# Optimization experiments

Measured on AMD Instinct MI355X. Metric: run time of the kernel, lower is better.

## Reference

```python
import jax, jax.numpy as jnp
import numpy as np

N, E, C, D, H = 50000, 1600000, 50000, 128, 512


def setup_inputs() -> dict:
    key = jax.random.key(0)
    ks = jax.random.split(key, 16)
    s = jnp.float32(0.02)  # keep activations stable through 3 layers
    inp = {}
    inp["x"] = jax.random.normal(ks[0], (N, D), jnp.float32)
    inp["edge_index"] = jax.random.randint(ks[1], (2, E), 0, N)
    inp["first_edge"] = jax.random.randint(ks[2], (2,), 0, N)
    inp["candidate_edges"] = jax.random.randint(ks[3], (C, 2), 0, N)
    inp["t"] = jax.random.uniform(ks[4], (1, 1), jnp.float32)
    dims = [(D, H), (H, H), (H, H)]
    i = 5
    for l, (di, do) in enumerate(dims):
        inp[f"gin{l}_w1"] = jax.random.normal(ks[i], (di, do), jnp.float32) * s; i += 1
        inp[f"gin{l}_b1"] = jnp.zeros((do,), jnp.float32)
        inp[f"gin{l}_w2"] = jax.random.normal(ks[i], (do, do), jnp.float32) * s; i += 1
        inp[f"gin{l}_b2"] = jnp.zeros((do,), jnp.float32)
    inp["pred_w1"] = jax.random.normal(ks[i], (5 * H, H), jnp.float32) * s; i += 1
    inp["pred_b1"] = jnp.zeros((H,), jnp.float32)
    inp["pred_w2"] = jax.random.normal(ks[i], (H, 1), jnp.float32) * s; i += 1
    inp["pred_b2"] = jnp.zeros((1,), jnp.float32)
    inp["time_w1"] = jax.random.normal(ks[i], (1, H), jnp.float32) * s; i += 1
    inp["time_b1"] = jnp.zeros((H,), jnp.float32)
    inp["time_w2"] = jax.random.normal(ks[i], (H, H), jnp.float32) * s; i += 1
    inp["time_b2"] = jnp.zeros((H,), jnp.float32)
    return inp


def _edge_rep(x, u, v):
    # 'sum_absdiff': cat([x_u + x_v, |x_u - x_v|]) -> 2*H features
    xu, xv = x[u], x[v]
    return jnp.concatenate([xu + xv, jnp.abs(xu - xv)], axis=-1)


def reference(x, edge_index, first_edge, candidate_edges, t,
              gin0_w1, gin0_b1, gin0_w2, gin0_b2,
              gin1_w1, gin1_b1, gin1_w2, gin1_b2,
              gin2_w1, gin2_b1, gin2_w2, gin2_b2,
              pred_w1, pred_b1, pred_w2, pred_b2,
              time_w1, time_b1, time_w2, time_b2):
    src, dst = edge_index[0], edge_index[1]
    layers = [(gin0_w1, gin0_b1, gin0_w2, gin0_b2),
              (gin1_w1, gin1_b1, gin1_w2, gin1_b2),
              (gin2_w1, gin2_b1, gin2_w2, gin2_b2)]
    # GINConv (eps=0): h_i = MLP(x_i + sum_{j->i} x_j)
    for w1, b1, w2, b2 in layers:
        agg = jax.ops.segment_sum(x[src], dst, num_segments=x.shape[0])
        h = x + agg
        x = jax.nn.relu(h @ w1 + b1) @ w2 + b2
    first_feat = _edge_rep(x, first_edge[0], first_edge[1])  # [2H]
    t_embed = (jax.nn.relu(t @ time_w1 + time_b1) @ time_w2 + time_b2)[0]  # [H]
    cand_feat = _edge_rep(x, candidate_edges[:, 0], candidate_edges[:, 1])  # [C, 2H]
    Cn = cand_feat.shape[0]
    feat = jnp.concatenate([
        jnp.broadcast_to(first_feat, (Cn, first_feat.shape[0])),
        cand_feat,
        jnp.broadcast_to(t_embed, (Cn, t_embed.shape[0])),
    ], axis=-1)  # [C, 5H]
    logits = (jax.nn.relu(feat @ pred_w1 + pred_b1) @ pred_w2 + pred_b2)[:, 0]  # [C]
    return logits
```

## Files before the change

kernel.cpp:

```cpp
#include <hip/hip_runtime.h>

typedef __bf16 bf16x2 __attribute__((ext_vector_type(2)));
typedef __bf16 bf16x4 __attribute__((ext_vector_type(4)));
typedef __bf16 bf16x8 __attribute__((ext_vector_type(8)));
typedef float f32x4 __attribute__((ext_vector_type(4)));

#define CSR_CHUNKS 256

__device__ __forceinline__ void gload16(const __bf16* g, __bf16* l) {
    __builtin_amdgcn_global_load_lds((const __attribute__((address_space(1))) void*)g,
                                     (__attribute__((address_space(3))) void*)l, 16, 0, 0);
}

__global__ __launch_bounds__(256)
void hist_part_kernel(const int* __restrict__ dst, int* __restrict__ deg, int E, int N) {
    const int r = blockIdx.x & 7;
    const int chunk = blockIdx.x >> 3;
    const int RS = (N + 7) >> 3;
    const int lo = r * RS;
    const int hi = min(lo + RS, N);
    const int stride = CSR_CHUNKS * 256;
    for (int i = chunk * 256 + threadIdx.x; i < E; i += stride) {
        int d = dst[i];
        if (d >= lo && d < hi) atomicAdd(&deg[d], 1);
    }
}

__global__ __launch_bounds__(256)
void scatter_part_kernel(const int* __restrict__ src, const int* __restrict__ dst,
                         int* __restrict__ cursor, int* __restrict__ colsrc, int E, int N) {
    const int r = blockIdx.x & 7;
    const int chunk = blockIdx.x >> 3;
    const int RS = (N + 7) >> 3;
    const int lo = r * RS;
    const int hi = min(lo + RS, N);
    const int stride = CSR_CHUNKS * 256;
    for (int i = chunk * 256 + threadIdx.x; i < E; i += stride) {
        int d = dst[i];
        if (d >= lo && d < hi) {
            int p = atomicAdd(&cursor[d], 1);
            colsrc[p] = src[i];
        }
    }
}

__global__ __launch_bounds__(256)
void blocksum_kernel(const int* __restrict__ deg, int* __restrict__ bsum, int n) {
    __shared__ int red[256];
    int i = blockIdx.x * 256 + threadIdx.x;
    red[threadIdx.x] = (i < n) ? deg[i] : 0;
    __syncthreads();
    for (int off = 128; off > 0; off >>= 1) {
        if (threadIdx.x < off) red[threadIdx.x] += red[threadIdx.x + off];
        __syncthreads();
    }
    if (threadIdx.x == 0) bsum[blockIdx.x] = red[0];
}

__global__ __launch_bounds__(256)
void scanb_kernel(int* __restrict__ bsum, int nb) {
    __shared__ int s[256];
    int t = threadIdx.x;
    s[t] = (t < nb) ? bsum[t] : 0;
    __syncthreads();
    for (int off = 1; off < 256; off <<= 1) {
        int v = (t >= off) ? s[t - off] : 0;
        __syncthreads();
        s[t] += v;
        __syncthreads();
    }
    if (t < nb) bsum[t] = (t == 0) ? 0 : s[t - 1];
}

__global__ __launch_bounds__(256)
void scanw_kernel(const int* __restrict__ deg, const int* __restrict__ bsum,
                  int* __restrict__ rowptr, int* __restrict__ cursor, int n) {
    __shared__ int s[256];
    int b = blockIdx.x, t = threadIdx.x;
    int i = b * 256 + t;
    int d = (i < n) ? deg[i] : 0;
    s[t] = d;
    __syncthreads();
    for (int off = 1; off < 256; off <<= 1) {
        int v = (t >= off) ? s[t - off] : 0;
        __syncthreads();
        s[t] += v;
        __syncthreads();
    }
    int incl = s[t];
    int base = bsum[b];
    if (i < n) {
        int r = base + incl - d;
        rowptr[i] = r;
        cursor[i] = r;
        if (i == n - 1) rowptr[n] = base + incl;
    }
}

__global__ void f32_to_bf16_kernel(const float* __restrict__ in, __bf16* __restrict__ out, int n4) {
    int i = blockIdx.x * 256 + threadIdx.x;
    if (i < n4) {
        float4 f = ((const float4*)in)[i];
        bf16x4 o;
        o[0] = (__bf16)f.x; o[1] = (__bf16)f.y; o[2] = (__bf16)f.z; o[3] = (__bf16)f.w;
        ((bf16x4*)out)[i] = o;
    }
}

__global__ void wprep_kernel(const float* __restrict__ in, __bf16* __restrict__ out, int kbits) {
    int idx = blockIdx.x * 256 + threadIdx.x;
    int K = 1 << kbits;
    if (idx < (512 << kbits)) {
        int k = idx & (K - 1);
        int n = idx >> kbits;
        out[idx] = (__bf16)in[k * 512 + n];
    }
}

template<int F> struct VecT;
template<> struct VecT<2> { using T = bf16x2; };
template<> struct VecT<4> { using T = bf16x4; };
template<> struct VecT<8> { using T = bf16x8; };

template<int F, int U, int STR>
__global__ __launch_bounds__(256)
void agg_kernel(const __bf16* __restrict__ xb, const int* __restrict__ rowptr,
                const int* __restrict__ colsrc, __bf16* __restrict__ h, int n, int colbase) {
    const int node = blockIdx.x * 4 + (threadIdx.x >> 6);
    if (node >= n) return;
    const int lane = threadIdx.x & 63;
    using V = typename VecT<F>::T;

    const __bf16* xl = xb + colbase + lane * F;

    float acc[F];
    {
        V v = *(const V*)(xl + (size_t)node * STR);
        #pragma unroll
        for (int i = 0; i < F; i++) acc[i] = (float)v[i];
    }

    int e   = __builtin_amdgcn_readfirstlane(rowptr[node]);
    int end = __builtin_amdgcn_readfirstlane(rowptr[node + 1]);

    for (; e + U <= end; e += U) {
        int s[U];
        #pragma unroll
        for (int j = 0; j < U; j++) s[j] = colsrc[e + j];
        V v[U];
        #pragma unroll
        for (int j = 0; j < U; j++) v[j] = *(const V*)(xl + (size_t)s[j] * STR);
        #pragma unroll
        for (int j = 0; j < U; j++)
            #pragma unroll
            for (int i = 0; i < F; i++) acc[i] += (float)v[j][i];
    }
    if constexpr (U > 4) {
        for (; e + 4 <= end; e += 4) {
            int s[4];
            #pragma unroll
            for (int j = 0; j < 4; j++) s[j] = colsrc[e + j];
            V v[4];
            #pragma unroll
            for (int j = 0; j < 4; j++) v[j] = *(const V*)(xl + (size_t)s[j] * STR);
            #pragma unroll
            for (int j = 0; j < 4; j++)
                #pragma unroll
                for (int i = 0; i < F; i++) acc[i] += (float)v[j][i];
        }
    }
    for (; e < end; e++) {
        int s0 = colsrc[e];
        V v = *(const V*)(xl + (size_t)s0 * STR);
        #pragma unroll
        for (int i = 0; i < F; i++) acc[i] += (float)v[i];
    }

    __bf16* out = h + colbase + (size_t)node * STR + lane * F;
    V o;
    #pragma unroll
    for (int i = 0; i < F; i++) o[i] = (__bf16)acc[i];
    *(V*)out = o;
}

template<bool RELU>
__global__ __launch_bounds__(512, 1)
void gemmF_kernel(const __bf16* __restrict__ A, const __bf16* __restrict__ Bt,
                  const float* __restrict__ bias, __bf16* __restrict__ Cout,
                  int M, int K) {
    __shared__ __bf16 smem[36864];
    __bf16* const sA0 = smem;
    __bf16* const sA1 = smem + 2048;
    __bf16* const sB0 = smem + 4096;
    __bf16* const sB1 = smem + 20480;

    const int tid = threadIdx.x;
    const int lane = tid & 63;
    const int wid = tid >> 6;
    const int mlane = lane & 15;
    const int quad = lane >> 4;
    const int rowBase = blockIdx.x * 64;

    const int swzc = (((lane & 3) ^ ((lane >> 3) & 3)) << 3);

    const int aRow = rowBase + wid * 16 + (lane >> 2);
    const int aRowC = (aRow < M) ? aRow : (M - 1);
    const __bf16* aSrc = A + (size_t)aRowC * K + swzc;
    const int bRow = wid * 64 + (lane >> 2);
    const __bf16* bSrc = Bt + (size_t)bRow * K + swzc;

    const int rkey = (mlane >> 1) & 3;
    const int base_r = mlane * 32 + ((quad ^ rkey) << 3);

    f32x4 acc[4][4];
    #pragma unroll
    for (int i = 0; i < 4; i++)
        #pragma unroll
        for (int j = 0; j < 4; j++) acc[i][j] = f32x4{0.f, 0.f, 0.f, 0.f};

    auto stage = [&](__bf16* bufA, __bf16* bufB, int k0) {
        if (wid < 4) gload16(aSrc + k0, bufA + wid * 512);
        #pragma unroll
        for (int j = 0; j < 4; j++)
            gload16(bSrc + (size_t)j * 16 * K + k0, bufB + wid * 2048 + j * 512);
    };
    auto waitc = [&]() {
        if (wid < 4) { asm volatile("s_waitcnt vmcnt(5)" ::: "memory"); }
        else         { asm volatile("s_waitcnt vmcnt(4)" ::: "memory"); }
    };
    auto compute = [&](const __bf16* bufA, const __bf16* bufB) {
        bf16x8 aF[4], bF[4];
        #pragma unroll
        for (int mt = 0; mt < 4; mt++)
            aF[mt] = *(const bf16x8*)(bufA + mt * 512 + base_r);
        #pragma unroll
        for (int nt = 0; nt < 4; nt++)
            bF[nt] = *(const bf16x8*)(bufB + wid * 2048 + nt * 512 + base_r);
        #pragma unroll
        for (int mt = 0; mt < 4; mt++)
            #pragma unroll
            for (int nt = 0; nt < 4; nt++)
                acc[mt][nt] = __builtin_amdgcn_mfma_f32_16x16x32_bf16(aF[mt], bF[nt], acc[mt][nt], 0, 0, 0);
    };

    const int nt = K >> 5;
    stage(sA0, sB0, 0);
    __builtin_amdgcn_sched_barrier(0);
    stage(sA1, sB1, 32);
    waitc();
    __builtin_amdgcn_sched_barrier(0);
    __builtin_amdgcn_s_barrier();
    __builtin_amdgcn_sched_barrier(0);

    int cur = 0;
    for (int t = 0; t < nt; ++t) {
        __bf16* cA = cur ? sA1 : sA0;
        __bf16* cB = cur ? sB1 : sB0;
        compute(cA, cB);
        if (t + 1 < nt) {
            __builtin_amdgcn_s_barrier();
            __builtin_amdgcn_sched_barrier(0);
            if (t + 2 < nt) {
                stage(cA, cB, (t + 2) << 5);
                waitc();
            } else {
                asm volatile("s_waitcnt vmcnt(0)" ::: "memory");
            }
            __builtin_amdgcn_sched_barrier(0);
            __builtin_amdgcn_s_barrier();
            __builtin_amdgcn_sched_barrier(0);
            cur ^= 1;
        }
    }

    float bv[4];
    #pragma unroll
    for (int nt2 = 0; nt2 < 4; nt2++) bv[nt2] = bias[wid * 64 + nt2 * 16 + mlane];

    float* tp = (float*)smem;
    const int erow = tid >> 5;
    const int ecg = tid & 31;
    #pragma unroll
    for (int mt = 0; mt < 4; mt++) {
        __syncthreads();
        #pragma unroll
        for (int nt2 = 0; nt2 < 4; nt2++) {
            #pragma unroll
            for (int r = 0; r < 4; r++) {
                float v = acc[mt][nt2][r] + bv[nt2];
                if (RELU) v = fmaxf(v, 0.f);
                tp[(quad * 4 + r) * 520 + wid * 64 + nt2 * 16 + mlane] = v;
            }
        }
        __syncthreads();
        int gr = rowBase + mt * 16 + erow;
        if (gr < M) {
            const float* rp = tp + erow * 520 + ecg * 16;
            f32x4 a = *(const f32x4*)(rp);
            f32x4 b = *(const f32x4*)(rp + 4);
            f32x4 c = *(const f32x4*)(rp + 8);
            f32x4 d = *(const f32x4*)(rp + 12);
            bf16x8 o0, o1;
            #pragma unroll
            for (int j = 0; j < 4; j++) { o0[j] = (__bf16)a[j]; o0[4 + j] = (__bf16)b[j]; }
            #pragma unroll
            for (int j = 0; j < 4; j++) { o1[j] = (__bf16)c[j]; o1[4 + j] = (__bf16)d[j]; }
            __bf16* op = Cout + (size_t)gr * 512 + ecg * 16;
            *(bf16x8*)op = o0;
            *(bf16x8*)(op + 8) = o1;
        }
    }
}

template<int AMODE, bool RELU>
__global__ __launch_bounds__(256, 3)
void gemm_kernel(const __bf16* __restrict__ A, const __bf16* __restrict__ Xb,
                 const int* __restrict__ cand, const __bf16* __restrict__ Bt,
                 const float* __restrict__ bias, __bf16* __restrict__ Cout,
                 int M, int K) {
    __shared__ __bf16 smem[2 * (2048 + 8192)];
    __bf16* const sA0 = smem;
    __bf16* const sA1 = smem + 2048;
    __bf16* const sB0 = smem + 4096;
    __bf16* const sB1 = smem + 4096 + 8192;

    const int bx = blockIdx.x;
    const int rblk = (bx >> 4) * 8 + (bx & 7);
    const int panel = (bx >> 3) & 1;
    const int rowBase = rblk * 64;
    if (rowBase >= M) return;
    const int nBase = panel * 256;

    const int tid = threadIdx.x;
    const int lane = tid & 63;
    const int wid = tid >> 6;
    const int mlane = lane & 15;
    const int quad = lane >> 4;

    const int swzc = (((lane & 3) ^ ((lane >> 3) & 3)) << 3);
    const int bRow = nBase + wid * 64 + (lane >> 2);
    const __bf16* bSrc = Bt + (size_t)bRow * K + swzc;

    const int rkey = (mlane >> 1) & 3;
    const int base_r = mlane * 32 + ((quad ^ rkey) << 3);

    const int ar = tid >> 2;
    const int acn = tid & 3;
    const int ac = acn << 3;
    const int wkey = (ar >> 1) & 3;
    const int woffA = ar * 32 + ((acn ^ wkey) << 3);

    f32x4 acc[4][4];
    #pragma unroll
    for (int i = 0; i < 4; i++)
        #pragma unroll
        for (int j = 0; j < 4; j++) acc[i][j] = f32x4{0.f, 0.f, 0.f, 0.f};

    int uu = 0, vv = 0;
    const int grow = rowBase + ar;
    const bool arowok = (grow < M);
    if (AMODE == 1 && arowok) { uu = cand[2 * grow]; vv = cand[2 * grow + 1]; }

    bf16x8 pxu{}, pxv{};
    int pk = 0;

    auto stageB = [&](__bf16* bufB, int k0) {
        #pragma unroll
        for (int j = 0; j < 4; j++)
            gload16(bSrc + (size_t)j * 16 * K + k0, bufB + wid * 2048 + j * 512);
    };
    auto issueA1 = [&](int k0) {
        pk = k0;
        if (arowok) {
            int kk = (k0 + ac) & 511;
            pxu = *(const bf16x8*)(Xb + (size_t)uu * 512 + kk);
            pxv = *(const bf16x8*)(Xb + (size_t)vv * 512 + kk);
        }
    };
    auto commitA1 = [&](__bf16* bufA) {
        bf16x8 av = bf16x8{};
        if (arowok) {
            if (pk + ac < 512) {
                #pragma unroll
                for (int q = 0; q < 8; q++) av[q] = (__bf16)((float)pxu[q] + (float)pxv[q]);
            } else {
                #pragma unroll
                for (int q = 0; q < 8; q++) av[q] = (__bf16)fabsf((float)pxu[q] - (float)pxv[q]);
            }
        }
        *(bf16x8*)(bufA + woffA) = av;
    };

    auto compute = [&](const __bf16* bufA, const __bf16* bufB) {
        bf16x8 aF[4], bF[4];
        #pragma unroll
        for (int mt = 0; mt < 4; mt++)
            aF[mt] = *(const bf16x8*)(bufA + mt * 512 + base_r);
        #pragma unroll
        for (int nt = 0; nt < 4; nt++)
            bF[nt] = *(const bf16x8*)(bufB + wid * 2048 + nt * 512 + base_r);
        #pragma unroll
        for (int mt = 0; mt < 4; mt++)
            #pragma unroll
            for (int nt = 0; nt < 4; nt++)
                acc[mt][nt] = __builtin_amdgcn_mfma_f32_16x16x32_bf16(aF[mt], bF[nt], acc[mt][nt], 0, 0, 0);
    };

    const int nt = K >> 5;
    issueA1(0);
    commitA1(sA0);
    stageB(sB0, 0);
    __syncthreads();
    for (int t = 0; t < nt; t += 2) {
        issueA1((t + 1) << 5);
        stageB(sB1, (t + 1) << 5);
        compute(sA0, sB0);
        commitA1(sA1);
        __syncthreads();
        if (t + 2 < nt) {
            issueA1((t + 2) << 5);
            stageB(sB0, (t + 2) << 5);
        }
        compute(sA1, sB1);
        if (t + 2 < nt) commitA1(sA0);
        __syncthreads();
    }

    float bv[4];
    #pragma unroll
    for (int nt2 = 0; nt2 < 4; nt2++) bv[nt2] = bias[nBase + wid * 64 + nt2 * 16 + mlane];

    float* tp = (float*)smem;
    const int erow = tid >> 4;
    const int ecg = tid & 15;
    #pragma unroll
    for (int mt = 0; mt < 4; mt++) {
        __syncthreads();
        #pragma unroll
        for (int nt2 = 0; nt2 < 4; nt2++) {
            #pragma unroll
            for (int r = 0; r < 4; r++) {
                float v = acc[mt][nt2][r] + bv[nt2];
                if (RELU) v = fmaxf(v, 0.f);
                tp[(quad * 4 + r) * 260 + wid * 64 + nt2 * 16 + mlane] = v;
            }
        }
        __syncthreads();
        int gr = rowBase + mt * 16 + erow;
        if (gr < M) {
            const float* rp = tp + erow * 260 + ecg * 16;
            f32x4 a = *(const f32x4*)(rp);
            f32x4 b = *(const f32x4*)(rp + 4);
            f32x4 c = *(const f32x4*)(rp + 8);
            f32x4 d = *(const f32x4*)(rp + 12);
            bf16x8 o0, o1;
            #pragma unroll
            for (int j = 0; j < 4; j++) { o0[j] = (__bf16)a[j]; o0[4 + j] = (__bf16)b[j]; }
            #pragma unroll
            for (int j = 0; j < 4; j++) { o1[j] = (__bf16)c[j]; o1[4 + j] = (__bf16)d[j]; }
            __bf16* op = Cout + (size_t)gr * 512 + nBase + ecg * 16;
            *(bf16x8*)op = o0;
            *(bf16x8*)(op + 8) = o1;
        }
    }
}

__global__ __launch_bounds__(512)
void constvec_kernel(const __bf16* __restrict__ xb, const int* __restrict__ first_edge,
                     const float* __restrict__ t,
                     const float* __restrict__ tw1, const float* __restrict__ tb1,
                     const float* __restrict__ tw2, const float* __restrict__ tb2,
                     const float* __restrict__ pw1, const float* __restrict__ pb1,
                     float* __restrict__ cvec) {
    __shared__ float z1[512];
    __shared__ float te[512];
    __shared__ float ff[1024];
    int tid = threadIdx.x;
    float tv = t[0];
    z1[tid] = fmaxf(tv * tw1[tid] + tb1[tid], 0.f);
    int u = first_edge[0], v = first_edge[1];
    float xu = (float)xb[(size_t)u * 512 + tid];
    float xv = (float)xb[(size_t)v * 512 + tid];
    ff[tid] = xu + xv;
    ff[512 + tid] = fabsf(xu - xv);
    __syncthreads();
    float s = tb2[tid];
    for (int j = 0; j < 512; j++) s += z1[j] * tw2[j * 512 + tid];
    te[tid] = s;
    __syncthreads();
    float c = pb1[tid];
    for (int k = 0; k < 1024; k++) c += ff[k] * pw1[k * 512 + tid];
    for (int j = 0; j < 512; j++) c += te[j] * pw1[(2048 + j) * 512 + tid];
    cvec[tid] = c;
}

__global__ __launch_bounds__(256)
void logits_kernel(const __bf16* __restrict__ Z, const float* __restrict__ w2,
                   const float* __restrict__ b2, float* __restrict__ out, int C) {
    int c = blockIdx.x * 4 + (threadIdx.x >> 6);
    if (c >= C) return;
    int lane = threadIdx.x & 63;
    bf16x8 z = *(const bf16x8*)(Z + (size_t)c * 512 + lane * 8);
    const float4* w = (const float4*)(w2 + lane * 8);
    float4 w0 = w[0], w1 = w[1];
    float s = (float)z[0] * w0.x + (float)z[1] * w0.y + (float)z[2] * w0.z + (float)z[3] * w0.w
            + (float)z[4] * w1.x + (float)z[5] * w1.y + (float)z[6] * w1.z + (float)z[7] * w1.w;
    #pragma unroll
    for (int off = 32; off > 0; off >>= 1) s += __shfl_down(s, off);
    if (lane == 0) out[c] = s + b2[0];
}

extern "C" void kernel_launch(void* const* d_in, const int* in_sizes, int n_in,
                              void* d_out, int out_size, void* d_ws, size_t ws_size,
                              hipStream_t stream) {
    (void)n_in; (void)out_size; (void)ws_size;
    const float* x          = (const float*)d_in[0];
    const int*   edge_index = (const int*)d_in[1];
    const int*   first_edge = (const int*)d_in[2];
    const int*   cand       = (const int*)d_in[3];
    const float* t          = (const float*)d_in[4];
    const float* gw1[3] = {(const float*)d_in[5], (const float*)d_in[9],  (const float*)d_in[13]};
    const float* gb1[3] = {(const float*)d_in[6], (const float*)d_in[10], (const float*)d_in[14]};
    const float* gw2[3] = {(const float*)d_in[7], (const float*)d_in[11], (const float*)d_in[15]};
    const float* gb2[3] = {(const float*)d_in[8], (const float*)d_in[12], (const float*)d_in[16]};
    const float* pw1 = (const float*)d_in[17];
    const float* pb1 = (const float*)d_in[18];
    const float* pw2 = (const float*)d_in[19];
    const float* pb2 = (const float*)d_in[20];
    const float* tw1 = (const float*)d_in[21];
    const float* tb1 = (const float*)d_in[22];
    const float* tw2 = (const float*)d_in[23];
    const float* tb2 = (const float*)d_in[24];

    const int N = in_sizes[0] / 128;
    const int E = in_sizes[1] / 2;
    const int C = in_sizes[3] / 2;

    char* p = (char*)d_ws;
    auto alloc = [&](size_t bytes) -> void* {
        void* r = (void*)p;
        p += (bytes + 255) & ~(size_t)255;
        return r;
    };
    __bf16* h    = (__bf16*)alloc((size_t)N * 512 * 2);
    __bf16* u    = (__bf16*)alloc((size_t)N * 512 * 2);
    __bf16* xb   = (__bf16*)alloc((size_t)N * 512 * 2);
    __bf16* wt01 = (__bf16*)alloc((size_t)512 * 128 * 2);
    __bf16* wt02 = (__bf16*)alloc((size_t)512 * 512 * 2);
    __bf16* wt11 = (__bf16*)alloc((size_t)512 * 512 * 2);
    __bf16* wt12 = (__bf16*)alloc((size_t)512 * 512 * 2);
    __bf16* wt21 = (__bf16*)alloc((size_t)512 * 512 * 2);
    __bf16* wt22 = (__bf16*)alloc((size_t)512 * 512 * 2);
    __bf16* wtH  = (__bf16*)alloc((size_t)512 * 1024 * 2);
    int* rowptr = (int*)alloc((size_t)(N + 1) * 4);
    int* deg    = (int*)alloc((size_t)N * 4);
    int* cursor = (int*)alloc((size_t)N * 4);
    int* colsrc = (int*)alloc((size_t)E * 4);
    int* bsum   = (int*)alloc((size_t)256 * 4);
    float* cvec = (float*)alloc(512 * 4);
    __bf16* xb0 = (__bf16*)u;

    const int* src = edge_index;
    const int* dst = edge_index + E;

    hipMemsetAsync(deg, 0, (size_t)N * 4, stream);
    int nb = (N + 255) / 256;
    hist_part_kernel<<<CSR_CHUNKS * 8, 256, 0, stream>>>(dst, deg, E, N);
    blocksum_kernel<<<nb, 256, 0, stream>>>(deg, bsum, N);
    scanb_kernel<<<1, 256, 0, stream>>>(bsum, nb);
    scanw_kernel<<<nb, 256, 0, stream>>>(deg, bsum, rowptr, cursor, N);
    scatter_part_kernel<<<CSR_CHUNKS * 8, 256, 0, stream>>>(src, dst, cursor, colsrc, E, N);

    f32_to_bf16_kernel<<<((N * 128 / 4) + 255) / 256, 256, 0, stream>>>(x, xb0, N * 128 / 4);
    wprep_kernel<<<((512 << 7)  + 255) / 256, 256, 0, stream>>>(gw1[0], wt01, 7);
    wprep_kernel<<<((512 << 9)  + 255) / 256, 256, 0, stream>>>(gw2[0], wt02, 9);
    wprep_kernel<<<((512 << 9)  + 255) / 256, 256, 0, stream>>>(gw1[1], wt11, 9);
    wprep_kernel<<<((512 << 9)  + 255) / 256, 256, 0, stream>>>(gw2[1], wt12, 9);
    wprep_kernel<<<((512 << 9)  + 255) / 256, 256, 0, stream>>>(gw1[2], wt21, 9);
    wprep_kernel<<<((512 << 9)  + 255) / 256, 256, 0, stream>>>(gw2[2], wt22, 9);
    wprep_kernel<<<((512 << 10) + 255) / 256, 256, 0, stream>>>(pw1 + (size_t)1024 * 512, wtH, 10);

    const int Rblk = (N + 63) / 64;
    const int gpair = ((Rblk + 7) / 8) * 16;
    int ablocks = (N + 3) / 4;

    agg_kernel<2, 16, 128><<<ablocks, 256, 0, stream>>>(xb0, rowptr, colsrc, h, N, 0);
    gemmF_kernel<true ><<<Rblk, 512, 0, stream>>>(h, wt01, gb1[0], u,  N, 128);
    gemmF_kernel<false><<<Rblk, 512, 0, stream>>>(u, wt02, gb2[0], xb, N, 512);
    agg_kernel<4, 8, 512><<<ablocks, 256, 0, stream>>>(xb, rowptr, colsrc, h, N, 0);
    agg_kernel<4, 8, 512><<<ablocks, 256, 0, stream>>>(xb, rowptr, colsrc, h, N, 256);
    gemmF_kernel<true ><<<Rblk, 512, 0, stream>>>(h, wt11, gb1[1], u,  N, 512);
    gemmF_kernel<false><<<Rblk, 512, 0, stream>>>(u, wt12, gb2[1], xb, N, 512);
    agg_kernel<4, 8, 512><<<ablocks, 256, 0, stream>>>(xb, rowptr, colsrc, h, N, 0);
    agg_kernel<4, 8, 512><<<ablocks, 256, 0, stream>>>(xb, rowptr, colsrc, h, N, 256);
    gemmF_kernel<true ><<<Rblk, 512, 0, stream>>>(h, wt21, gb1[2], u,  N, 512);
    gemmF_kernel<false><<<Rblk, 512, 0, stream>>>(u, wt22, gb2[2], xb, N, 512);

    constvec_kernel<<<1, 512, 0, stream>>>(xb, first_edge, t, tw1, tb1, tw2, tb2, pw1, pb1, cvec);
    gemm_kernel<1, true><<<gpair, 256, 0, stream>>>(nullptr, xb, cand, wtH, cvec, u, C, 1024);
    logits_kernel<<<(C + 3) / 4, 256, 0, stream>>>(u, pw2, pb2, (float*)d_out, C);
}
```

Before: 1.227 ms.

## Fuse each GIN layer's two GEMMs into one kernel keeping hidden tile in LDS

Replaces the two per-layer GEMM launches (Linear+ReLU, then Linear) with one kernel that computes the 64x512 hidden tile, applies bias and ReLU, and writes it as bf16 into a swizzled LDS buffer. The second GEMM then reads its A operand from LDS and streams only the second weight matrix. This removes the global write and re-read of the intermediate activation and one launch per layer. In exchange each block uses about 136KB of LDS, which caps occupancy at one block per CU and serialises the two GEMM phases inside the block.

```diff
diff --git a/kernel.cpp b/kernel.cpp
--- a/kernel.cpp
+++ b/kernel.cpp
@@ -183,16 +183,19 @@
     *(V*)out = o;
 }
 
-template<bool RELU>
+template<int DUMMY>
 __global__ __launch_bounds__(512, 1)
-void gemmF_kernel(const __bf16* __restrict__ A, const __bf16* __restrict__ Bt,
-                  const float* __restrict__ bias, __bf16* __restrict__ Cout,
-                  int M, int K) {
-    __shared__ __bf16 smem[36864];
-    __bf16* const sA0 = smem;
-    __bf16* const sA1 = smem + 2048;
-    __bf16* const sB0 = smem + 4096;
-    __bf16* const sB1 = smem + 20480;
+void layer_kernel(const __bf16* __restrict__ A, const __bf16* __restrict__ B1t,
+                  const float* __restrict__ b1, const __bf16* __restrict__ B2t,
+                  const float* __restrict__ b2, __bf16* __restrict__ Out,
+                  int M, int K1) {
+    __shared__ __bf16 smem[69760];
+    __bf16* const U   = smem;
+    __bf16* const sA0 = smem + 32896;
+    __bf16* const sA1 = smem + 34944;
+    __bf16* const sB0 = smem + 36992;
+    __bf16* const sB1 = smem + 53376;
+    float* const  tp  = (float*)(smem + 36992);
 
     const int tid = threadIdx.x;
     const int lane = tid & 63;
@@ -205,9 +208,10 @@
 
     const int aRow = rowBase + wid * 16 + (lane >> 2);
     const int aRowC = (aRow < M) ? aRow : (M - 1);
-    const __bf16* aSrc = A + (size_t)aRowC * K + swzc;
+    const __bf16* aSrc = A + (size_t)aRowC * K1 + swzc;
     const int bRow = wid * 64 + (lane >> 2);
-    const __bf16* bSrc = Bt + (size_t)bRow * K + swzc;
+    const __bf16* bSrc1 = B1t + (size_t)bRow * K1 + swzc;
+    const __bf16* bSrc2 = B2t + (size_t)bRow * 512 + swzc;
 
     const int rkey = (mlane >> 1) & 3;
     const int base_r = mlane * 32 + ((quad ^ rkey) << 3);
@@ -218,17 +222,22 @@
         #pragma unroll
         for (int j = 0; j < 4; j++) acc[i][j] = f32x4{0.f, 0.f, 0.f, 0.f};
 
-    auto stage = [&](__bf16* bufA, __bf16* bufB, int k0) {
+    auto stage1 = [&](__bf16* bufA, __bf16* bufB, int k0) {
         if (wid < 4) gload16(aSrc + k0, bufA + wid * 512);
         #pragma unroll
         for (int j = 0; j < 4; j++)
-            gload16(bSrc + (size_t)j * 16 * K + k0, bufB + wid * 2048 + j * 512);
-    };
-    auto waitc = [&]() {
+            gload16(bSrc1 + (size_t)j * 16 * K1 + k0, bufB + wid * 2048 + j * 512);
+    };
+    auto wait1 = [&]() {
         if (wid < 4) { asm volatile("s_waitcnt vmcnt(5)" ::: "memory"); }
         else         { asm volatile("s_waitcnt vmcnt(4)" ::: "memory"); }
     };
-    auto compute = [&](const __bf16* bufA, const __bf16* bufB) {
+    auto stage2 = [&](__bf16* bufB, int k0) {
+        #pragma unroll
+        for (int j = 0; j < 4; j++)
+            gload16(bSrc2 + (size_t)j * 16 * 512 + k0, bufB + wid * 2048 + j * 512);
+    };
+    auto computeAB = [&](const __bf16* bufA, const __bf16* bufB) {
         bf16x8 aF[4], bF[4];
         #pragma unroll
         for (int mt = 0; mt < 4; mt++)
@@ -242,27 +251,42 @@
             for (int nt = 0; nt < 4; nt++)
                 acc[mt][nt] = __builtin_amdgcn_mfma_f32_16x16x32_bf16(aF[mt], bF[nt], acc[mt][nt], 0, 0, 0);
     };
-
-    const int nt = K >> 5;
-    stage(sA0, sB0, 0);
+    auto computeU = [&](int t, const __bf16* bufB) {
+        const __bf16* pA = U + (size_t)t * 2056;
+        bf16x8 aF[4], bF[4];
+        #pragma unroll
+        for (int mt = 0; mt < 4; mt++)
+            aF[mt] = *(const bf16x8*)(pA + mt * 512 + base_r);
+        #pragma unroll
+        for (int nt = 0; nt < 4; nt++)
+            bF[nt] = *(const bf16x8*)(bufB + wid * 2048 + nt * 512 + base_r);
+        #pragma unroll
+        for (int mt = 0; mt < 4; mt++)
+            #pragma unroll
+            for (int nt = 0; nt < 4; nt++)
+                acc[mt][nt] = __builtin_amdgcn_mfma_f32_16x16x32_bf16(aF[mt], bF[nt], acc[mt][nt], 0, 0, 0);
+    };
+
+    const int nt1 = K1 >> 5;
+    stage1(sA0, sB0, 0);
     __builtin_amdgcn_sched_barrier(0);
-    stage(sA1, sB1, 32);
-    waitc();
+    stage1(sA1, sB1, 32);
+    wait1();
     __builtin_amdgcn_sched_barrier(0);
     __builtin_amdgcn_s_barrier();
     __builtin_amdgcn_sched_barrier(0);
 
     int cur = 0;
-    for (int t = 0; t < nt; ++t) {
+    for (int t = 0; t < nt1; ++t) {
         __bf16* cA = cur ? sA1 : sA0;
         __bf16* cB = cur ? sB1 : sB0;
-        compute(cA, cB);
-        if (t + 1 < nt) {
+        computeAB(cA, cB);
+        if (t + 1 < nt1) {
             __builtin_amdgcn_s_barrier();
             __builtin_amdgcn_sched_barrier(0);
-            if (t + 2 < nt) {
-                stage(cA, cB, (t + 2) << 5);
-                waitc();
+            if (t + 2 < nt1) {
+                stage1(cA, cB, (t + 2) << 5);
+                wait1();
             } else {
                 asm volatile("s_waitcnt vmcnt(0)" ::: "memory");
             }
@@ -273,29 +297,26 @@
         }
     }
 
-    float bv[4];
-    #pragma unroll
-    for (int nt2 = 0; nt2 < 4; nt2++) bv[nt2] = bias[wid * 64 + nt2 * 16 + mlane];
-
-    float* tp = (float*)smem;
-    const int erow = tid >> 5;
-    const int ecg = tid & 31;
-    #pragma unroll
-    for (int mt = 0; mt < 4; mt++) {
-        __syncthreads();
-        #pragma unroll
-        for (int nt2 = 0; nt2 < 4; nt2++) {
-            #pragma unroll
-            for (int r = 0; r < 4; r++) {
-                float v = acc[mt][nt2][r] + bv[nt2];
-                if (RELU) v = fmaxf(v, 0.f);
-                tp[(quad * 4 + r) * 520 + wid * 64 + nt2 * 16 + mlane] = v;
+    {
+        float bv[4];
+        #pragma unroll
+        for (int nt = 0; nt < 4; nt++) bv[nt] = b1[wid * 64 + nt * 16 + mlane];
+
+        const int erow = tid >> 5;
+        const int ecg = tid & 31;
+        #pragma unroll
+        for (int mt = 0; mt < 4; mt++) {
+            __syncthreads();
+            #pragma unroll
+            for (int nt = 0; nt < 4; nt++) {
+                #pragma unroll
+                for (int r = 0; r < 4; r++) {
+                    float v = fmaxf(acc[mt][nt][r] + bv[nt], 0.f);
+                    tp[(quad * 4 + r) * 516 + wid * 64 + nt * 16 + mlane] = v;
+                }
             }
-        }
-        __syncthreads();
-        int gr = rowBase + mt * 16 + erow;
-        if (gr < M) {
-            const float* rp = tp + erow * 520 + ecg * 16;
+            __syncthreads();
+            const float* rp = tp + erow * 516 + ecg * 16;
             f32x4 a = *(const f32x4*)(rp);
             f32x4 b = *(const f32x4*)(rp + 4);
             f32x4 c = *(const f32x4*)(rp + 8);
@@ -305,9 +326,83 @@
             for (int j = 0; j < 4; j++) { o0[j] = (__bf16)a[j]; o0[4 + j] = (__bf16)b[j]; }
             #pragma unroll
             for (int j = 0; j < 4; j++) { o1[j] = (__bf16)c[j]; o1[4 + j] = (__bf16)d[j]; }
-            __bf16* op = Cout + (size_t)gr * 512 + ecg * 16;
-            *(bf16x8*)op = o0;
-            *(bf16x8*)(op + 8) = o1;
+            const int r64 = mt * 16 + erow;
+            const int key = (r64 >> 1) & 3;
+            const int p = ecg >> 1;
+            const int c0 = (ecg & 1) << 1;
+            __bf16* up = U + (size_t)p * 2056 + r64 * 32;
+            *(bf16x8*)(up + ((c0 ^ key) << 3)) = o0;
+            *(bf16x8*)(up + (((c0 + 1) ^ key) << 3)) = o1;
+        }
+        __syncthreads();
+    }
+
+    #pragma unroll
+    for (int i = 0; i < 4; i++)
+        #pragma unroll
+        for (int j = 0; j < 4; j++) acc[i][j] = f32x4{0.f, 0.f, 0.f, 0.f};
+
+    stage2(sB0, 0);
+    __builtin_amdgcn_sched_barrier(0);
+    stage2(sB1, 32);
+    asm volatile("s_waitcnt vmcnt(4)" ::: "memory");
+    __builtin_amdgcn_sched_barrier(0);
+    __builtin_amdgcn_s_barrier();
+    __builtin_amdgcn_sched_barrier(0);
+
+    cur = 0;
+    for (int t = 0; t < 16; ++t) {
+        __bf16* cB = cur ? sB1 : sB0;
+        computeU(t, cB);
+        if (t + 1 < 16) {
+            __builtin_amdgcn_s_barrier();
+            __builtin_amdgcn_sched_barrier(0);
+            if (t + 2 < 16) {
+                stage2(cB, (t + 2) << 5);
+                asm volatile("s_waitcnt vmcnt(4)" ::: "memory");
+            } else {
+                asm volatile("s_waitcnt vmcnt(0)" ::: "memory");
+            }
+            __builtin_amdgcn_sched_barrier(0);
+            __builtin_amdgcn_s_barrier();
+            __builtin_amdgcn_sched_barrier(0);
+            cur ^= 1;
+        }
+    }
+
+    {
+        float bv[4];
+        #pragma unroll
+        for (int nt = 0; nt < 4; nt++) bv[nt] = b2[wid * 64 + nt * 16 + mlane];
+
+        const int erow = tid >> 5;
+        const int ecg = tid & 31;
+        #pragma unroll
+        for (int mt = 0; mt < 4; mt++) {
+            __syncthreads();
+            #pragma unroll
+            for (int nt = 0; nt < 4; nt++) {
+                #pragma unroll
+                for (int r = 0; r < 4; r++)
+                    tp[(quad * 4 + r) * 516 + wid * 64 + nt * 16 + mlane] = acc[mt][nt][r] + bv[nt];
+            }
+            __syncthreads();
+            int gr = rowBase + mt * 16 + erow;
+            if (gr < M) {
+                const float* rp = tp + erow * 516 + ecg * 16;
+                f32x4 a = *(const f32x4*)(rp);
+                f32x4 b = *(const f32x4*)(rp + 4);
+                f32x4 c = *(const f32x4*)(rp + 8);
+                f32x4 d = *(const f32x4*)(rp + 12);
+                bf16x8 o0, o1;
+                #pragma unroll
+                for (int j = 0; j < 4; j++) { o0[j] = (__bf16)a[j]; o0[4 + j] = (__bf16)b[j]; }
+                #pragma unroll
+                for (int j = 0; j < 4; j++) { o1[j] = (__bf16)c[j]; o1[4 + j] = (__bf16)d[j]; }
+                __bf16* op = Out + (size_t)gr * 512 + ecg * 16;
+                *(bf16x8*)op = o0;
+                *(bf16x8*)(op + 8) = o1;
+            }
         }
     }
 }
@@ -585,16 +680,13 @@
     int ablocks = (N + 3) / 4;
 
     agg_kernel<2, 16, 128><<<ablocks, 256, 0, stream>>>(xb0, rowptr, colsrc, h, N, 0);
-    gemmF_kernel<true ><<<Rblk, 512, 0, stream>>>(h, wt01, gb1[0], u,  N, 128);
-    gemmF_kernel<false><<<Rblk, 512, 0, stream>>>(u, wt02, gb2[0], xb, N, 512);
+    layer_kernel<0><<<Rblk, 512, 0, stream>>>(h, wt01, gb1[0], wt02, gb2[0], xb, N, 128);
     agg_kernel<4, 8, 512><<<ablocks, 256, 0, stream>>>(xb, rowptr, colsrc, h, N, 0);
     agg_kernel<4, 8, 512><<<ablocks, 256, 0, stream>>>(xb, rowptr, colsrc, h, N, 256);
-    gemmF_kernel<true ><<<Rblk, 512, 0, stream>>>(h, wt11, gb1[1], u,  N, 512);
-    gemmF_kernel<false><<<Rblk, 512, 0, stream>>>(u, wt12, gb2[1], xb, N, 512);
+    layer_kernel<0><<<Rblk, 512, 0, stream>>>(h, wt11, gb1[1], wt12, gb2[1], xb, N, 512);
     agg_kernel<4, 8, 512><<<ablocks, 256, 0, stream>>>(xb, rowptr, colsrc, h, N, 0);
     agg_kernel<4, 8, 512><<<ablocks, 256, 0, stream>>>(xb, rowptr, colsrc, h, N, 256);
-    gemmF_kernel<true ><<<Rblk, 512, 0, stream>>>(h, wt21, gb1[2], u,  N, 512);
-    gemmF_kernel<false><<<Rblk, 512, 0, stream>>>(u, wt22, gb2[2], xb, N, 512);
+    layer_kernel<0><<<Rblk, 512, 0, stream>>>(h, wt21, gb1[2], wt22, gb2[2], xb, N, 512);
 
     constvec_kernel<<<1, 512, 0, stream>>>(xb, first_edge, t, tw1, tb1, tw2, tb2, pw1, pb1, cvec);
     gemm_kernel<1, true><<<gpair, 256, 0, stream>>>(nullptr, xb, cand, wtH, cvec, u, C, 1024);
```

New measurement: 1.230 ms. Within noise of the previous version (+0.2%).
